# Optimization experiments

Hardware: AMD Instinct MI355X
Metric: run time of the kernel (lower is better)

## Reference

```python
import jax, jax.numpy as jnp
import numpy as np

V, E, H = 32000, 512, 1024
B, T = 16, 256
EPS = 1e-5

def setup_inputs() -> dict:
    key = jax.random.key(0)
    ks = jax.random.split(key, 20)
    s = lambda *shape: 0.02
    inp = {
        'input': jax.random.randint(ks[0], (B, T), 0, V),
        'embd': jax.random.normal(ks[1], (V, E), jnp.float32) * 0.02,
        # layer 0 GRUCell (input E -> H)
        'Wih0': jax.random.normal(ks[2], (3 * H, E), jnp.float32) * 0.02,
        'Whh0': jax.random.normal(ks[3], (3 * H, H), jnp.float32) * 0.02,
        'bih0': jnp.zeros((3 * H,), jnp.float32),
        'bhh0': jnp.zeros((3 * H,), jnp.float32),
        'ln0_w': jnp.ones((H,), jnp.float32),
        'ln0_b': jnp.zeros((H,), jnp.float32),
        # layer 1 GRUCell (H -> H)
        'Wih1': jax.random.normal(ks[4], (3 * H, H), jnp.float32) * 0.02,
        'Whh1': jax.random.normal(ks[5], (3 * H, H), jnp.float32) * 0.02,
        'bih1': jnp.zeros((3 * H,), jnp.float32),
        'bhh1': jnp.zeros((3 * H,), jnp.float32),
        'ln1_w': jnp.ones((H,), jnp.float32),
        'ln1_b': jnp.zeros((H,), jnp.float32),
        # head: Linear(H,H) -> LeakyReLU -> LayerNorm -> Linear(H,V)
        'W1': jax.random.normal(ks[6], (H, H), jnp.float32) * 0.02,
        'b1': jnp.zeros((H,), jnp.float32),
        'ln2_w': jnp.ones((H,), jnp.float32),
        'ln2_b': jnp.zeros((H,), jnp.float32),
        'W2': jax.random.normal(ks[7], (V, H), jnp.float32) * 0.02,
        'b2': jnp.zeros((V,), jnp.float32),
    }
    return inp

def _layernorm(x, w, b):
    m = jnp.mean(x, axis=-1, keepdims=True)
    v = jnp.var(x, axis=-1, keepdims=True)
    return (x - m) * jax.lax.rsqrt(v + EPS) * w + b

def _gru_cell(x, h, Wih, Whh, bih, bhh):
    gi = x @ Wih.T + bih  # [B, 3H]
    gh = h @ Whh.T + bhh
    ir, iz, inn = jnp.split(gi, 3, axis=-1)
    hr, hz, hn = jnp.split(gh, 3, axis=-1)
    r = jax.nn.sigmoid(ir + hr)
    z = jax.nn.sigmoid(iz + hz)
    n = jnp.tanh(inn + r * hn)
    return (1.0 - z) * n + z * h

def reference(input, embd, Wih0, Whh0, bih0, bhh0, ln0_w, ln0_b,
              Wih1, Whh1, bih1, bhh1, ln1_w, ln1_b,
              W1, b1, ln2_w, ln2_b, W2, b2):
    x = embd[input]                      # [B, T, E]
    xT = jnp.swapaxes(x, 0, 1)           # [T, B, E]
    Bn = input.shape[0]
    h0 = jnp.zeros((Bn, H), x.dtype)
    h1 = jnp.zeros((Bn, H), x.dtype)

    def step(carry, xt):
        h0, h1 = carry
        h0 = _layernorm(_gru_cell(xt, h0, Wih0, Whh0, bih0, bhh0), ln0_w, ln0_b)
        h1 = _layernorm(_gru_cell(h0, h1, Wih1, Whh1, bih1, bhh1), ln1_w, ln1_b)
        a = jax.nn.leaky_relu(h1 @ W1.T + b1, negative_slope=0.01)
        a = _layernorm(a, ln2_w, ln2_b)
        logits = a @ W2.T + b2           # [B, V]
        return (h0, h1), logits

    _, outs = jax.lax.scan(step, (h0, h1), xT)   # [T, B, V]
    return jnp.swapaxes(outs, 0, 1)              # [B, T, V]
```

## Files before the change

kernel.cpp:

```cpp
#include <hip/hip_runtime.h>
#include <stdint.h>
#include <math.h>

#define TT 256
#define VOCAB 32000
#define LN_EPS 1e-5

typedef __attribute__((ext_vector_type(8))) short bf16x8;
typedef __attribute__((ext_vector_type(4))) float f32x4;

__device__ __forceinline__ float bf2f(short s) {
  return __uint_as_float(((uint32_t)(uint16_t)s) << 16);
}
__device__ __forceinline__ short f2bf(float f) {
  uint32_t u = __float_as_uint(f);
  u += 0x7fffu + ((u >> 16) & 1u);
  return (short)(u >> 16);
}
__device__ __forceinline__ f32x4 mfma16(bf16x8 a, bf16x8 b, f32x4 c) {
  return __builtin_amdgcn_mfma_f32_16x16x32_bf16(a, b, c, 0, 0, 0);
}

__global__ void k_gi0(const int* __restrict__ input, const float* __restrict__ embd,
                      const float* __restrict__ Wih0, const float* __restrict__ bih0,
                      double* __restrict__ gi0) {
  const int t = blockIdx.x >> 4;
  const int cg = blockIdx.x & 15;
  const int tid = threadIdx.x;
  __shared__ float xs[16][512];
  for (int idx = tid; idx < 16 * 512; idx += 256) {
    const int r = idx >> 9, j = idx & 511;
    const int tok = input[r * TT + t];
    xs[r][j] = embd[(size_t)tok * 512 + j];
  }
  __syncthreads();
  const int row = tid >> 4, ct = tid & 15;
  for (int i = 0; i < 12; ++i) {
    const int c = cg * 192 + ct + 16 * i;
    const float4* wp = (const float4*)(Wih0 + (size_t)c * 512);
    const float4* xp = (const float4*)&xs[row][0];
    double acc = 0.0;
#pragma unroll 8
    for (int j4 = 0; j4 < 128; ++j4) {
      const float4 w = wp[j4];
      const float4 x = xp[j4];
      acc = fma((double)x.x, (double)w.x, acc);
      acc = fma((double)x.y, (double)w.y, acc);
      acc = fma((double)x.z, (double)w.z, acc);
      acc = fma((double)x.w, (double)w.w, acc);
    }
    gi0[((size_t)t * 16 + row) * 3072 + c] = acc + (double)bih0[c];
  }
}

struct SP {
  const float *Whh0, *bhh0, *ln0w, *ln0b;
  const float *Wih1, *Whh1, *bih1, *bhh1, *ln1w, *ln1b;
  const double* gi0;
  double *h0ring, *h1ring;
  float* h1hist;
  int p;
};

__launch_bounds__(512, 2)
__global__ void k_step(SP A) {
  __shared__ double sPre[16 * 16 * 3];
  __shared__ double sM[16], sR[16];
  const int tid = threadIdx.x;
  const int row = tid >> 5;
  const int ks = tid & 31;
  const int bid = blockIdx.x;

  if (bid < 64) {
    const int t = A.p;
    if (t >= TT) return;
    const int col0 = bid * 16;
    double a[32];
    if (t > 0) {
      const double* hp = A.h0ring + (size_t)((t - 1) & 1) * 16384 + row * 1024;
      double s = 0.0, q = 0.0;
#pragma unroll
      for (int g = 0; g < 8; ++g)
#pragma unroll
        for (int u = 0; u < 4; ++u) {
          const double v = hp[g * 128 + ks * 4 + u];
          a[g * 4 + u] = v; s += v; q += v * v;
        }
#pragma unroll
      for (int mk = 1; mk <= 16; mk <<= 1) { s += __shfl_xor(s, mk); q += __shfl_xor(q, mk); }
      const double m = s * (1.0 / 1024.0);
      const double rs = 1.0 / sqrt(q * (1.0 / 1024.0) - m * m + LN_EPS);
      if (ks == 0) { sM[row] = m; sR[row] = rs; }
#pragma unroll
      for (int g = 0; g < 8; ++g) {
        const float4 lw = *(const float4*)(A.ln0w + g * 128 + ks * 4);
        const float4 lb = *(const float4*)(A.ln0b + g * 128 + ks * 4);
        a[g * 4 + 0] = (a[g * 4 + 0] - m) * rs * (double)lw.x + (double)lb.x;
        a[g * 4 + 1] = (a[g * 4 + 1] - m) * rs * (double)lw.y + (double)lb.y;
        a[g * 4 + 2] = (a[g * 4 + 2] - m) * rs * (double)lw.z + (double)lb.z;
        a[g * 4 + 3] = (a[g * 4 + 3] - m) * rs * (double)lw.w + (double)lb.w;
      }
      for (int cc = 0; cc < 16; ++cc) {
        const int c = col0 + cc;
        const float4* pr = (const float4*)(A.Whh0 + (size_t)c * 1024);
        const float4* pz = (const float4*)(A.Whh0 + (size_t)(c + 1024) * 1024);
        const float4* pn = (const float4*)(A.Whh0 + (size_t)(c + 2048) * 1024);
        double ar = 0.0, az = 0.0, an_ = 0.0;
#pragma unroll
        for (int g = 0; g < 8; ++g) {
          const int o = g * 32 + ks;
          const float4 wr = pr[o], wz = pz[o], wn = pn[o];
          ar = fma(a[g*4+0], (double)wr.x, ar); ar = fma(a[g*4+1], (double)wr.y, ar);
          ar = fma(a[g*4+2], (double)wr.z, ar); ar = fma(a[g*4+3], (double)wr.w, ar);
          az = fma(a[g*4+0], (double)wz.x, az); az = fma(a[g*4+1], (double)wz.y, az);
          az = fma(a[g*4+2], (double)wz.z, az); az = fma(a[g*4+3], (double)wz.w, az);
          an_ = fma(a[g*4+0], (double)wn.x, an_); an_ = fma(a[g*4+1], (double)wn.y, an_);
          an_ = fma(a[g*4+2], (double)wn.z, an_); an_ = fma(a[g*4+3], (double)wn.w, an_);
        }
#pragma unroll
        for (int mk = 1; mk <= 16; mk <<= 1) {
          ar += __shfl_xor(ar, mk); az += __shfl_xor(az, mk); an_ += __shfl_xor(an_, mk);
        }
        if (ks == 0) {
          sPre[(row * 16 + cc) * 3 + 0] = ar;
          sPre[(row * 16 + cc) * 3 + 1] = az;
          sPre[(row * 16 + cc) * 3 + 2] = an_;
        }
      }
    } else {
      if (tid < 256) {
        sPre[tid * 3 + 0] = 0.0; sPre[tid * 3 + 1] = 0.0; sPre[tid * 3 + 2] = 0.0;
      }
    }
    __syncthreads();
    if (tid < 256) {
      const int r2 = tid >> 4, cc = tid & 15;
      const int c = col0 + cc;
      const double ghr = sPre[(r2 * 16 + cc) * 3 + 0] + (double)A.bhh0[c];
      const double ghz = sPre[(r2 * 16 + cc) * 3 + 1] + (double)A.bhh0[c + 1024];
      const double ghn = sPre[(r2 * 16 + cc) * 3 + 2] + (double)A.bhh0[c + 2048];
      const double* gp = A.gi0 + ((size_t)t * 16 + r2) * 3072 + c;
      const double gir = gp[0], giz = gp[1024], gin = gp[2048];
      const double rg = 1.0 / (1.0 + exp(-(gir + ghr)));
      const double zg = 1.0 / (1.0 + exp(-(giz + ghz)));
      const double ng = tanh(gin + rg * ghn);
      double hprev = 0.0;
      if (t > 0) {
        const double praw = A.h0ring[(size_t)((t - 1) & 1) * 16384 + r2 * 1024 + c];
        hprev = (praw - sM[r2]) * sR[r2] * (double)A.ln0w[c] + (double)A.ln0b[c];
      }
      A.h0ring[(size_t)(t & 1) * 16384 + r2 * 1024 + c] = (1.0 - zg) * ng + zg * hprev;
    }
  } else {
    const int t = A.p - 1;
    if (t < 0 || t >= TT) return;
    const int col0 = (bid - 64) * 8;
    double a0[32], a1[32];
    {
      const double* hp = A.h0ring + (size_t)(t & 1) * 16384 + row * 1024;
      double s = 0.0, q = 0.0;
#pragma unroll
      for (int g = 0; g < 8; ++g)
#pragma unroll
        for (int u = 0; u < 4; ++u) {
          const double v = hp[g * 128 + ks * 4 + u];
          a0[g * 4 + u] = v; s += v; q += v * v;
        }
#pragma unroll
      for (int mk = 1; mk <= 16; mk <<= 1) { s += __shfl_xor(s, mk); q += __shfl_xor(q, mk); }
      const double m = s * (1.0 / 1024.0);
      const double rs = 1.0 / sqrt(q * (1.0 / 1024.0) - m * m + LN_EPS);
#pragma unroll
      for (int g = 0; g < 8; ++g) {
        const float4 lw = *(const float4*)(A.ln0w + g * 128 + ks * 4);
        const float4 lb = *(const float4*)(A.ln0b + g * 128 + ks * 4);
        a0[g * 4 + 0] = (a0[g * 4 + 0] - m) * rs * (double)lw.x + (double)lb.x;
        a0[g * 4 + 1] = (a0[g * 4 + 1] - m) * rs * (double)lw.y + (double)lb.y;
        a0[g * 4 + 2] = (a0[g * 4 + 2] - m) * rs * (double)lw.z + (double)lb.z;
        a0[g * 4 + 3] = (a0[g * 4 + 3] - m) * rs * (double)lw.w + (double)lb.w;
      }
    }
    if (t > 0) {
      const double* hp = A.h1ring + (size_t)((t - 1) & 1) * 16384 + row * 1024;
      double s = 0.0, q = 0.0;
#pragma unroll
      for (int g = 0; g < 8; ++g)
#pragma unroll
        for (int u = 0; u < 4; ++u) {
          const double v = hp[g * 128 + ks * 4 + u];
          a1[g * 4 + u] = v; s += v; q += v * v;
        }
#pragma unroll
      for (int mk = 1; mk <= 16; mk <<= 1) { s += __shfl_xor(s, mk); q += __shfl_xor(q, mk); }
      const double m = s * (1.0 / 1024.0);
      const double rs = 1.0 / sqrt(q * (1.0 / 1024.0) - m * m + LN_EPS);
      if (ks == 0) { sM[row] = m; sR[row] = rs; }
#pragma unroll
      for (int g = 0; g < 8; ++g) {
        const float4 lw = *(const float4*)(A.ln1w + g * 128 + ks * 4);
        const float4 lb = *(const float4*)(A.ln1b + g * 128 + ks * 4);
        a1[g * 4 + 0] = (a1[g * 4 + 0] - m) * rs * (double)lw.x + (double)lb.x;
        a1[g * 4 + 1] = (a1[g * 4 + 1] - m) * rs * (double)lw.y + (double)lb.y;
        a1[g * 4 + 2] = (a1[g * 4 + 2] - m) * rs * (double)lw.z + (double)lb.z;
        a1[g * 4 + 3] = (a1[g * 4 + 3] - m) * rs * (double)lw.w + (double)lb.w;
      }
    } else {
#pragma unroll
      for (int j = 0; j < 32; ++j) a1[j] = 0.0;
    }
    for (int cc = 0; cc < 8; ++cc) {
      const int c = col0 + cc;
      const float4* ir = (const float4*)(A.Wih1 + (size_t)c * 1024);
      const float4* iz = (const float4*)(A.Wih1 + (size_t)(c + 1024) * 1024);
      const float4* in_ = (const float4*)(A.Wih1 + (size_t)(c + 2048) * 1024);
      const float4* hr = (const float4*)(A.Whh1 + (size_t)c * 1024);
      const float4* hz = (const float4*)(A.Whh1 + (size_t)(c + 1024) * 1024);
      const float4* hn = (const float4*)(A.Whh1 + (size_t)(c + 2048) * 1024);
      double sIr = 0.0, sIz = 0.0, sIn = 0.0, sHr = 0.0, sHz = 0.0, sHn = 0.0;
#pragma unroll
      for (int g = 0; g < 8; ++g) {
        const int o = g * 32 + ks;
        const float4 w0 = ir[o], w1 = iz[o], w2 = in_[o];
        const float4 w3 = hr[o], w4 = hz[o], w5 = hn[o];
        sIr = fma(a0[g*4+0], (double)w0.x, sIr); sIr = fma(a0[g*4+1], (double)w0.y, sIr);
        sIr = fma(a0[g*4+2], (double)w0.z, sIr); sIr = fma(a0[g*4+3], (double)w0.w, sIr);
        sIz = fma(a0[g*4+0], (double)w1.x, sIz); sIz = fma(a0[g*4+1], (double)w1.y, sIz);
        sIz = fma(a0[g*4+2], (double)w1.z, sIz); sIz = fma(a0[g*4+3], (double)w1.w, sIz);
        sIn = fma(a0[g*4+0], (double)w2.x, sIn); sIn = fma(a0[g*4+1], (double)w2.y, sIn);
        sIn = fma(a0[g*4+2], (double)w2.z, sIn); sIn = fma(a0[g*4+3], (double)w2.w, sIn);
        sHr = fma(a1[g*4+0], (double)w3.x, sHr); sHr = fma(a1[g*4+1], (double)w3.y, sHr);
        sHr = fma(a1[g*4+2], (double)w3.z, sHr); sHr = fma(a1[g*4+3], (double)w3.w, sHr);
        sHz = fma(a1[g*4+0], (double)w4.x, sHz); sHz = fma(a1[g*4+1], (double)w4.y, sHz);
        sHz = fma(a1[g*4+2], (double)w4.z, sHz); sHz = fma(a1[g*4+3], (double)w4.w, sHz);
        sHn = fma(a1[g*4+0], (double)w5.x, sHn); sHn = fma(a1[g*4+1], (double)w5.y, sHn);
        sHn = fma(a1[g*4+2], (double)w5.z, sHn); sHn = fma(a1[g*4+3], (double)w5.w, sHn);
      }
#pragma unroll
      for (int mk = 1; mk <= 16; mk <<= 1) {
        sIr += __shfl_xor(sIr, mk); sIz += __shfl_xor(sIz, mk); sIn += __shfl_xor(sIn, mk);
        sHr += __shfl_xor(sHr, mk); sHz += __shfl_xor(sHz, mk); sHn += __shfl_xor(sHn, mk);
      }
      if (ks == 0) {
        double* pp = &sPre[(row * 8 + cc) * 6];
        pp[0] = sIr; pp[1] = sIz; pp[2] = sIn; pp[3] = sHr; pp[4] = sHz; pp[5] = sHn;
      }
    }
    __syncthreads();
    if (tid < 128) {
      const int r2 = tid >> 3, cc = tid & 7;
      const int c = col0 + cc;
      const double* pp = &sPre[(r2 * 8 + cc) * 6];
      const double gir = pp[0] + (double)A.bih1[c];
      const double giz = pp[1] + (double)A.bih1[c + 1024];
      const double gin = pp[2] + (double)A.bih1[c + 2048];
      const double ghr = pp[3] + (double)A.bhh1[c];
      const double ghz = pp[4] + (double)A.bhh1[c + 1024];
      const double ghn = pp[5] + (double)A.bhh1[c + 2048];
      const double rg = 1.0 / (1.0 + exp(-(gir + ghr)));
      const double zg = 1.0 / (1.0 + exp(-(giz + ghz)));
      const double ng = tanh(gin + rg * ghn);
      double hprev = 0.0;
      if (t > 0) {
        const double praw = A.h1ring[(size_t)((t - 1) & 1) * 16384 + r2 * 1024 + c];
        hprev = (praw - sM[r2]) * sR[r2] * (double)A.ln1w[c] + (double)A.ln1b[c];
      }
      const double hnew = (1.0 - zg) * ng + zg * hprev;
      A.h1ring[(size_t)(t & 1) * 16384 + r2 * 1024 + c] = hnew;
      A.h1hist[((size_t)t * 16 + r2) * 1024 + c] = (float)hnew;
    }
  }
}

__launch_bounds__(512, 2)
__global__ void k_headpre(const float* __restrict__ h1hist, const float* __restrict__ ln1w,
                          const float* __restrict__ ln1b, const float* __restrict__ W1,
                          const float* __restrict__ b1, short* __restrict__ araw) {
  const int tid = threadIdx.x;
  const int row = tid >> 5, ks = tid & 31;
  const size_t m = (size_t)blockIdx.x * 16 + row;
  const float* hp = h1hist + m * 1024;
  float a[32];
  float s = 0.f, q = 0.f;
#pragma unroll
  for (int g = 0; g < 8; ++g) {
    const float4 v = *(const float4*)(hp + g * 128 + ks * 4);
    a[g*4+0] = v.x; a[g*4+1] = v.y; a[g*4+2] = v.z; a[g*4+3] = v.w;
    s += v.x + v.y + v.z + v.w;
    q += v.x * v.x + v.y * v.y + v.z * v.z + v.w * v.w;
  }
#pragma unroll
  for (int mk = 1; mk <= 16; mk <<= 1) { s += __shfl_xor(s, mk); q += __shfl_xor(q, mk); }
  const float mn = s * (1.f / 1024.f);
  const float rs = rsqrtf(q * (1.f / 1024.f) - mn * mn + 1e-5f);
#pragma unroll
  for (int g = 0; g < 8; ++g) {
    const float4 lw = *(const float4*)(ln1w + g * 128 + ks * 4);
    const float4 lb = *(const float4*)(ln1b + g * 128 + ks * 4);
    a[g*4+0] = (a[g*4+0] - mn) * rs * lw.x + lb.x;
    a[g*4+1] = (a[g*4+1] - mn) * rs * lw.y + lb.y;
    a[g*4+2] = (a[g*4+2] - mn) * rs * lw.z + lb.z;
    a[g*4+3] = (a[g*4+3] - mn) * rs * lw.w + lb.w;
  }
  for (int c = 0; c < 1024; ++c) {
    const float4* wp = (const float4*)(W1 + (size_t)c * 1024);
    float acc = 0.f;
#pragma unroll
    for (int g = 0; g < 8; ++g) {
      const float4 w = wp[g * 32 + ks];
      acc = fmaf(a[g*4+0], w.x, acc); acc = fmaf(a[g*4+1], w.y, acc);
      acc = fmaf(a[g*4+2], w.z, acc); acc = fmaf(a[g*4+3], w.w, acc);
    }
#pragma unroll
    for (int mk = 1; mk <= 16; mk <<= 1) acc += __shfl_xor(acc, mk);
    if (ks == 0) {
      const float y = acc + b1[c];
      araw[m * 1024 + c] = f2bf(y > 0.f ? y : 0.01f * y);
    }
  }
}

__global__ void k_head(const short* __restrict__ araw, const float* __restrict__ W2,
                       const float* __restrict__ ln2w, const float* __restrict__ ln2b,
                       const float* __restrict__ b2, float* __restrict__ C) {
  __shared__ __align__(16) short As[128 * 64];
  __shared__ __align__(16) short Bs[128 * 64];
  __shared__ float rowm[128], rowr[128];
  __shared__ float lnw_s[1024], lnb_s[1024];
  __shared__ float ps[256], pq[256];
  const int tid = threadIdx.x;
  const long brow = (long)blockIdx.y * 128;
  const long bcol = (long)blockIdx.x * 128;

  for (int i = tid; i < 1024; i += 256) { lnw_s[i] = ln2w[i]; lnb_s[i] = ln2b[i]; }
  {
    const int r2 = tid >> 1, hf = tid & 1;
    const short* ap = araw + (brow + r2) * 1024 + hf * 512;
    float s = 0.f, q = 0.f;
    for (int j = 0; j < 512; j += 8) {
      const bf16x8 v = *(const bf16x8*)(ap + j);
#pragma unroll
      for (int e = 0; e < 8; ++e) { const float x = bf2f(v[e]); s += x; q += x * x; }
    }
    ps[tid] = s; pq[tid] = q;
  }
  __syncthreads();
  if (tid < 128) {
    const float s = ps[2 * tid] + ps[2 * tid + 1];
    const float q = pq[2 * tid] + pq[2 * tid + 1];
    const float m = s * (1.f / 1024.f);
    rowm[tid] = m;
    rowr[tid] = rsqrtf(q * (1.f / 1024.f) - m * m + 1e-5f);
  }
  __syncthreads();

  const int l = tid & 63;
  const int w = tid >> 6;
  const int wm = w >> 1, wn = w & 1;
  const int lane15 = l & 15, lgrp = l >> 4;
  f32x4 zero4 = {0.f, 0.f, 0.f, 0.f};
  f32x4 acc[4][4];
#pragma unroll
  for (int ri = 0; ri < 4; ++ri)
#pragma unroll
    for (int ci = 0; ci < 4; ++ci) acc[ri][ci] = zero4;

  for (int k0 = 0; k0 < 1024; k0 += 64) {
    __syncthreads();
#pragma unroll
    for (int i = 0; i < 4; ++i) {
      const int c = tid + i * 256;
      const int r = c >> 3, cc = c & 7;
      const int k = k0 + cc * 8;
      {
        const bf16x8 v = *(const bf16x8*)(araw + (brow + r) * 1024 + k);
        const float mm = rowm[r], rr = rowr[r];
        bf16x8 o;
#pragma unroll
        for (int e = 0; e < 8; ++e)
          o[e] = f2bf((bf2f(v[e]) - mm) * rr * lnw_s[k + e] + lnb_s[k + e]);
        *(bf16x8*)&As[r * 64 + cc * 8] = o;
      }
      {
        const float4* bp = (const float4*)(W2 + (bcol + r) * 1024 + k);
        const float4 v0 = bp[0], v1 = bp[1];
        bf16x8 o;
        o[0] = f2bf(v0.x); o[1] = f2bf(v0.y); o[2] = f2bf(v0.z); o[3] = f2bf(v0.w);
        o[4] = f2bf(v1.x); o[5] = f2bf(v1.y); o[6] = f2bf(v1.z); o[7] = f2bf(v1.w);
        *(bf16x8*)&Bs[r * 64 + cc * 8] = o;
      }
    }
    __syncthreads();
#pragma unroll
    for (int kk = 0; kk < 2; ++kk) {
      const int ko = kk * 32 + lgrp * 8;
      bf16x8 av[4], bv[4];
#pragma unroll
      for (int ri = 0; ri < 4; ++ri) av[ri] = *(const bf16x8*)&As[(wm * 64 + ri * 16 + lane15) * 64 + ko];
#pragma unroll
      for (int ci = 0; ci < 4; ++ci) bv[ci] = *(const bf16x8*)&Bs[(wn * 64 + ci * 16 + lane15) * 64 + ko];
#pragma unroll
      for (int ri = 0; ri < 4; ++ri)
#pragma unroll
        for (int ci = 0; ci < 4; ++ci) acc[ri][ci] = mfma16(av[ri], bv[ci], acc[ri][ci]);
    }
  }
#pragma unroll
  for (int ri = 0; ri < 4; ++ri)
#pragma unroll
    for (int ci = 0; ci < 4; ++ci)
#pragma unroll
      for (int i = 0; i < 4; ++i) {
        const long mrow = brow + wm * 64 + ri * 16 + lgrp * 4 + i;
        const long ncol = bcol + wn * 64 + ci * 16 + lane15;
        const int tq = (int)(mrow >> 4), b = (int)(mrow & 15);
        C[(size_t)b * TT * VOCAB + (size_t)tq * VOCAB + ncol] = acc[ri][ci][i] + b2[ncol];
      }
}

extern "C" void kernel_launch(void* const* d_in, const int* in_sizes, int n_in,
                              void* d_out, int out_size, void* d_ws, size_t ws_size,
                              hipStream_t stream) {
  const int* input = (const int*)d_in[0];
  const float* embd = (const float*)d_in[1];
  const float* Wih0 = (const float*)d_in[2];
  const float* Whh0 = (const float*)d_in[3];
  const float* bih0 = (const float*)d_in[4];
  const float* bhh0 = (const float*)d_in[5];
  const float* ln0w = (const float*)d_in[6];
  const float* ln0b = (const float*)d_in[7];
  const float* Wih1 = (const float*)d_in[8];
  const float* Whh1 = (const float*)d_in[9];
  const float* bih1 = (const float*)d_in[10];
  const float* bhh1 = (const float*)d_in[11];
  const float* ln1w = (const float*)d_in[12];
  const float* ln1b = (const float*)d_in[13];
  const float* W1 = (const float*)d_in[14];
  const float* b1 = (const float*)d_in[15];
  const float* ln2w = (const float*)d_in[16];
  const float* ln2b = (const float*)d_in[17];
  const float* W2 = (const float*)d_in[18];
  const float* b2 = (const float*)d_in[19];
  float* out = (float*)d_out;

  char* ws = (char*)d_ws;
  size_t off = 0;
  auto alloc = [&](size_t bytes) -> char* {
    char* p = ws + off;
    off = (off + bytes + 255) & ~(size_t)255;
    return p;
  };
  double* h0ring = (double*)alloc(2ull * 16 * 1024 * 8);
  double* h1ring = (double*)alloc(2ull * 16 * 1024 * 8);
  float* h1hist = (float*)alloc(4096ull * 1024 * 4);
  short* araw = (short*)alloc(4096ull * 1024 * 2);

  double* gi0 = (double*)d_out;

  k_gi0<<<4096, 256, 0, stream>>>(input, embd, Wih0, bih0, gi0);

  SP A;
  A.Whh0 = Whh0; A.bhh0 = bhh0; A.ln0w = ln0w; A.ln0b = ln0b;
  A.Wih1 = Wih1; A.Whh1 = Whh1; A.bih1 = bih1; A.bhh1 = bhh1;
  A.ln1w = ln1w; A.ln1b = ln1b;
  A.gi0 = gi0; A.h0ring = h0ring; A.h1ring = h1ring; A.h1hist = h1hist;
  for (int p = 0; p <= TT; ++p) {
    A.p = p;
    k_step<<<192, 512, 0, stream>>>(A);
  }

  k_headpre<<<256, 512, 0, stream>>>(h1hist, ln1w, ln1b, W1, b1, araw);

  k_head<<<dim3(250, 32), 256, 0, stream>>>(araw, W2, ln2w, ln2b, b2, out);
}
```

Measured before the change: 15.92 ms.

## Replace per-step kernel launches with persistent kernel and grid-wide atomic barrier

```diff
diff --git a/kernel.cpp b/kernel.cpp
--- a/kernel.cpp
+++ b/kernel.cpp
@@ -5,6 +5,7 @@
 #define TT 256
 #define VOCAB 32000
 #define LN_EPS 1e-5
+#define NBLK 192
 
 typedef __attribute__((ext_vector_type(8))) short bf16x8;
 typedef __attribute__((ext_vector_type(4))) float f32x4;
@@ -59,11 +60,11 @@
   const double* gi0;
   double *h0ring, *h1ring;
   float* h1hist;
-  int p;
+  int* bar;
 };
 
-__launch_bounds__(512, 2)
-__global__ void k_step(SP A) {
+__launch_bounds__(512, 1)
+__global__ void k_recur(SP A) {
   __shared__ double sPre[16 * 16 * 3];
   __shared__ double sM[16], sR[16];
   const int tid = threadIdx.x;
@@ -71,203 +72,219 @@
   const int ks = tid & 31;
   const int bid = blockIdx.x;
 
-  if (bid < 64) {
-    const int t = A.p;
-    if (t >= TT) return;
-    const int col0 = bid * 16;
-    double a[32];
-    if (t > 0) {
-      const double* hp = A.h0ring + (size_t)((t - 1) & 1) * 16384 + row * 1024;
-      double s = 0.0, q = 0.0;
-#pragma unroll
-      for (int g = 0; g < 8; ++g)
-#pragma unroll
-        for (int u = 0; u < 4; ++u) {
-          const double v = hp[g * 128 + ks * 4 + u];
-          a[g * 4 + u] = v; s += v; q += v * v;
-        }
-#pragma unroll
-      for (int mk = 1; mk <= 16; mk <<= 1) { s += __shfl_xor(s, mk); q += __shfl_xor(q, mk); }
-      const double m = s * (1.0 / 1024.0);
-      const double rs = 1.0 / sqrt(q * (1.0 / 1024.0) - m * m + LN_EPS);
-      if (ks == 0) { sM[row] = m; sR[row] = rs; }
-#pragma unroll
-      for (int g = 0; g < 8; ++g) {
-        const float4 lw = *(const float4*)(A.ln0w + g * 128 + ks * 4);
-        const float4 lb = *(const float4*)(A.ln0b + g * 128 + ks * 4);
-        a[g * 4 + 0] = (a[g * 4 + 0] - m) * rs * (double)lw.x + (double)lb.x;
-        a[g * 4 + 1] = (a[g * 4 + 1] - m) * rs * (double)lw.y + (double)lb.y;
-        a[g * 4 + 2] = (a[g * 4 + 2] - m) * rs * (double)lw.z + (double)lb.z;
-        a[g * 4 + 3] = (a[g * 4 + 3] - m) * rs * (double)lw.w + (double)lb.w;
-      }
-      for (int cc = 0; cc < 16; ++cc) {
-        const int c = col0 + cc;
-        const float4* pr = (const float4*)(A.Whh0 + (size_t)c * 1024);
-        const float4* pz = (const float4*)(A.Whh0 + (size_t)(c + 1024) * 1024);
-        const float4* pn = (const float4*)(A.Whh0 + (size_t)(c + 2048) * 1024);
-        double ar = 0.0, az = 0.0, an_ = 0.0;
-#pragma unroll
-        for (int g = 0; g < 8; ++g) {
-          const int o = g * 32 + ks;
-          const float4 wr = pr[o], wz = pz[o], wn = pn[o];
-          ar = fma(a[g*4+0], (double)wr.x, ar); ar = fma(a[g*4+1], (double)wr.y, ar);
-          ar = fma(a[g*4+2], (double)wr.z, ar); ar = fma(a[g*4+3], (double)wr.w, ar);
-          az = fma(a[g*4+0], (double)wz.x, az); az = fma(a[g*4+1], (double)wz.y, az);
-          az = fma(a[g*4+2], (double)wz.z, az); az = fma(a[g*4+3], (double)wz.w, az);
-          an_ = fma(a[g*4+0], (double)wn.x, an_); an_ = fma(a[g*4+1], (double)wn.y, an_);
-          an_ = fma(a[g*4+2], (double)wn.z, an_); an_ = fma(a[g*4+3], (double)wn.w, an_);
-        }
-#pragma unroll
-        for (int mk = 1; mk <= 16; mk <<= 1) {
-          ar += __shfl_xor(ar, mk); az += __shfl_xor(az, mk); an_ += __shfl_xor(an_, mk);
-        }
-        if (ks == 0) {
-          sPre[(row * 16 + cc) * 3 + 0] = ar;
-          sPre[(row * 16 + cc) * 3 + 1] = az;
-          sPre[(row * 16 + cc) * 3 + 2] = an_;
+  for (int p = 0; p <= TT; ++p) {
+    if (bid < 64) {
+      const int t = p;
+      if (t < TT) {
+        const int col0 = bid * 16;
+        double a[32];
+        if (t > 0) {
+          const double* hp = A.h0ring + (size_t)((t - 1) & 1) * 16384 + row * 1024;
+          double s = 0.0, q = 0.0;
+#pragma unroll
+          for (int g = 0; g < 8; ++g)
+#pragma unroll
+            for (int u = 0; u < 4; ++u) {
+              const double v = hp[g * 128 + ks * 4 + u];
+              a[g * 4 + u] = v; s += v; q += v * v;
+            }
+#pragma unroll
+          for (int mk = 1; mk <= 16; mk <<= 1) { s += __shfl_xor(s, mk); q += __shfl_xor(q, mk); }
+          const double m = s * (1.0 / 1024.0);
+          const double rs = 1.0 / sqrt(q * (1.0 / 1024.0) - m * m + LN_EPS);
+          if (ks == 0) { sM[row] = m; sR[row] = rs; }
+#pragma unroll
+          for (int g = 0; g < 8; ++g) {
+            const float4 lw = *(const float4*)(A.ln0w + g * 128 + ks * 4);
+            const float4 lb = *(const float4*)(A.ln0b + g * 128 + ks * 4);
+            a[g * 4 + 0] = (a[g * 4 + 0] - m) * rs * (double)lw.x + (double)lb.x;
+            a[g * 4 + 1] = (a[g * 4 + 1] - m) * rs * (double)lw.y + (double)lb.y;
+            a[g * 4 + 2] = (a[g * 4 + 2] - m) * rs * (double)lw.z + (double)lb.z;
+            a[g * 4 + 3] = (a[g * 4 + 3] - m) * rs * (double)lw.w + (double)lb.w;
+          }
+          for (int cc = 0; cc < 16; ++cc) {
+            const int c = col0 + cc;
+            const float4* pr = (const float4*)(A.Whh0 + (size_t)c * 1024);
+            const float4* pz = (const float4*)(A.Whh0 + (size_t)(c + 1024) * 1024);
+            const float4* pn = (const float4*)(A.Whh0 + (size_t)(c + 2048) * 1024);
+            double ar = 0.0, az = 0.0, an_ = 0.0;
+#pragma unroll
+            for (int g = 0; g < 8; ++g) {
+              const int o = g * 32 + ks;
+              const float4 wr = pr[o], wz = pz[o], wn = pn[o];
+              ar = fma(a[g*4+0], (double)wr.x, ar); ar = fma(a[g*4+1], (double)wr.y, ar);
+              ar = fma(a[g*4+2], (double)wr.z, ar); ar = fma(a[g*4+3], (double)wr.w, ar);
+              az = fma(a[g*4+0], (double)wz.x, az); az = fma(a[g*4+1], (double)wz.y, az);
+              az = fma(a[g*4+2], (double)wz.z, az); az = fma(a[g*4+3], (double)wz.w, az);
+              an_ = fma(a[g*4+0], (double)wn.x, an_); an_ = fma(a[g*4+1], (double)wn.y, an_);
+              an_ = fma(a[g*4+2], (double)wn.z, an_); an_ = fma(a[g*4+3], (double)wn.w, an_);
+            }
+#pragma unroll
+            for (int mk = 1; mk <= 16; mk <<= 1) {
+              ar += __shfl_xor(ar, mk); az += __shfl_xor(az, mk); an_ += __shfl_xor(an_, mk);
+            }
+            if (ks == 0) {
+              sPre[(row * 16 + cc) * 3 + 0] = ar;
+              sPre[(row * 16 + cc) * 3 + 1] = az;
+              sPre[(row * 16 + cc) * 3 + 2] = an_;
+            }
+          }
+        } else {
+          if (tid < 256) {
+            sPre[tid * 3 + 0] = 0.0; sPre[tid * 3 + 1] = 0.0; sPre[tid * 3 + 2] = 0.0;
+          }
+        }
+        __syncthreads();
+        if (tid < 256) {
+          const int r2 = tid >> 4, cc = tid & 15;
+          const int c = col0 + cc;
+          const double ghr = sPre[(r2 * 16 + cc) * 3 + 0] + (double)A.bhh0[c];
+          const double ghz = sPre[(r2 * 16 + cc) * 3 + 1] + (double)A.bhh0[c + 1024];
+          const double ghn = sPre[(r2 * 16 + cc) * 3 + 2] + (double)A.bhh0[c + 2048];
+          const double* gp = A.gi0 + ((size_t)t * 16 + r2) * 3072 + c;
+          const double gir = gp[0], giz = gp[1024], gin = gp[2048];
+          const double rg = 1.0 / (1.0 + exp(-(gir + ghr)));
+          const double zg = 1.0 / (1.0 + exp(-(giz + ghz)));
+          const double ng = tanh(gin + rg * ghn);
+          double hprev = 0.0;
+          if (t > 0) {
+            const double praw = A.h0ring[(size_t)((t - 1) & 1) * 16384 + r2 * 1024 + c];
+            hprev = (praw - sM[r2]) * sR[r2] * (double)A.ln0w[c] + (double)A.ln0b[c];
+          }
+          A.h0ring[(size_t)(t & 1) * 16384 + r2 * 1024 + c] = (1.0 - zg) * ng + zg * hprev;
         }
       }
     } else {
-      if (tid < 256) {
-        sPre[tid * 3 + 0] = 0.0; sPre[tid * 3 + 1] = 0.0; sPre[tid * 3 + 2] = 0.0;
-      }
-    }
+      const int t = p - 1;
+      if (t >= 0 && t < TT) {
+        const int col0 = (bid - 64) * 8;
+        double a0[32], a1[32];
+        {
+          const double* hp = A.h0ring + (size_t)(t & 1) * 16384 + row * 1024;
+          double s = 0.0, q = 0.0;
+#pragma unroll
+          for (int g = 0; g < 8; ++g)
+#pragma unroll
+            for (int u = 0; u < 4; ++u) {
+              const double v = hp[g * 128 + ks * 4 + u];
+              a0[g * 4 + u] = v; s += v; q += v * v;
+            }
+#pragma unroll
+          for (int mk = 1; mk <= 16; mk <<= 1) { s += __shfl_xor(s, mk); q += __shfl_xor(q, mk); }
+          const double m = s * (1.0 / 1024.0);
+          const double rs = 1.0 / sqrt(q * (1.0 / 1024.0) - m * m + LN_EPS);
+#pragma unroll
+          for (int g = 0; g < 8; ++g) {
+            const float4 lw = *(const float4*)(A.ln0w + g * 128 + ks * 4);
+            const float4 lb = *(const float4*)(A.ln0b + g * 128 + ks * 4);
+            a0[g * 4 + 0] = (a0[g * 4 + 0] - m) * rs * (double)lw.x + (double)lb.x;
+            a0[g * 4 + 1] = (a0[g * 4 + 1] - m) * rs * (double)lw.y + (double)lb.y;
+            a0[g * 4 + 2] = (a0[g * 4 + 2] - m) * rs * (double)lw.z + (double)lb.z;
+            a0[g * 4 + 3] = (a0[g * 4 + 3] - m) * rs * (double)lw.w + (double)lb.w;
+          }
+        }
+        if (t > 0) {
+          const double* hp = A.h1ring + (size_t)((t - 1) & 1) * 16384 + row * 1024;
+          double s = 0.0, q = 0.0;
+#pragma unroll
+          for (int g = 0; g < 8; ++g)
+#pragma unroll
+            for (int u = 0; u < 4; ++u) {
+              const double v = hp[g * 128 + ks * 4 + u];
+              a1[g * 4 + u] = v; s += v; q += v * v;
+            }
+#pragma unroll
+          for (int mk = 1; mk <= 16; mk <<= 1) { s += __shfl_xor(s, mk); q += __shfl_xor(q, mk); }
+          const double m = s * (1.0 / 1024.0);
+          const double rs = 1.0 / sqrt(q * (1.0 / 1024.0) - m * m + LN_EPS);
+          if (ks == 0) { sM[row] = m; sR[row] = rs; }
+#pragma unroll
+          for (int g = 0; g < 8; ++g) {
+            const float4 lw = *(const float4*)(A.ln1w + g * 128 + ks * 4);
+            const float4 lb = *(const float4*)(A.ln1b + g * 128 + ks * 4);
+            a1[g * 4 + 0] = (a1[g * 4 + 0] - m) * rs * (double)lw.x + (double)lb.x;
+            a1[g * 4 + 1] = (a1[g * 4 + 1] - m) * rs * (double)lw.y + (double)lb.y;
+            a1[g * 4 + 2] = (a1[g * 4 + 2] - m) * rs * (double)lw.z + (double)lb.z;
+            a1[g * 4 + 3] = (a1[g * 4 + 3] - m) * rs * (double)lw.w + (double)lb.w;
+          }
+        } else {
+#pragma unroll
+          for (int j = 0; j < 32; ++j) a1[j] = 0.0;
+        }
+        for (int cc = 0; cc < 8; ++cc) {
+          const int c = col0 + cc;
+          const float4* ir = (const float4*)(A.Wih1 + (size_t)c * 1024);
+          const float4* iz = (const float4*)(A.Wih1 + (size_t)(c + 1024) * 1024);
+          const float4* in_ = (const float4*)(A.Wih1 + (size_t)(c + 2048) * 1024);
+          const float4* hr = (const float4*)(A.Whh1 + (size_t)c * 1024);
+          const float4* hz = (const float4*)(A.Whh1 + (size_t)(c + 1024) * 1024);
+          const float4* hn = (const float4*)(A.Whh1 + (size_t)(c + 2048) * 1024);
+          double sIr = 0.0, sIz = 0.0, sIn = 0.0, sHr = 0.0, sHz = 0.0, sHn = 0.0;
+#pragma unroll
+          for (int g = 0; g < 8; ++g) {
+            const int o = g * 32 + ks;
+            const float4 w0 = ir[o], w1 = iz[o], w2 = in_[o];
+            const float4 w3 = hr[o], w4 = hz[o], w5 = hn[o];
+            sIr = fma(a0[g*4+0], (double)w0.x, sIr); sIr = fma(a0[g*4+1], (double)w0.y, sIr);
+            sIr = fma(a0[g*4+2], (double)w0.z, sIr); sIr = fma(a0[g*4+3], (double)w0.w, sIr);
+            sIz = fma(a0[g*4+0], (double)w1.x, sIz); sIz = fma(a0[g*4+1], (double)w1.y, sIz);
+            sIz = fma(a0[g*4+2], (double)w1.z, sIz); sIz = fma(a0[g*4+3], (double)w1.w, sIz);
+            sIn = fma(a0[g*4+0], (double)w2.x, sIn); sIn = fma(a0[g*4+1], (double)w2.y, sIn);
+            sIn = fma(a0[g*4+2], (double)w2.z, sIn); sIn = fma(a0[g*4+3], (double)w2.w, sIn);
+            sHr = fma(a1[g*4+0], (double)w3.x, sHr); sHr = fma(a1[g*4+1], (double)w3.y, sHr);
+            sHr = fma(a1[g*4+2], (double)w3.z, sHr); sHr = fma(a1[g*4+3], (double)w3.w, sHr);
+            sHz = fma(a1[g*4+0], (double)w4.x, sHz); sHz = fma(a1[g*4+1], (double)w4.y, sHz);
+            sHz = fma(a1[g*4+2], (double)w4.z, sHz); sHz = fma(a1[g*4+3], (double)w4.w, sHz);
+            sHn = fma(a1[g*4+0], (double)w5.x, sHn); sHn = fma(a1[g*4+1], (double)w5.y, sHn);
+            sHn = fma(a1[g*4+2], (double)w5.z, sHn); sHn = fma(a1[g*4+3], (double)w5.w, sHn);
+          }
+#pragma unroll
+          for (int mk = 1; mk <= 16; mk <<= 1) {
+            sIr += __shfl_xor(sIr, mk); sIz += __shfl_xor(sIz, mk); sIn += __shfl_xor(sIn, mk);
+            sHr += __shfl_xor(sHr, mk); sHz += __shfl_xor(sHz, mk); sHn += __shfl_xor(sHn, mk);
+          }
+          if (ks == 0) {
+            double* pp = &sPre[(row * 8 + cc) * 6];
+            pp[0] = sIr; pp[1] = sIz; pp[2] = sIn; pp[3] = sHr; pp[4] = sHz; pp[5] = sHn;
+          }
+        }
+        __syncthreads();
+        if (tid < 128) {
+          const int r2 = tid >> 3, cc = tid & 7;
+          const int c = col0 + cc;
+          const double* pp = &sPre[(r2 * 8 + cc) * 6];
+          const double gir = pp[0] + (double)A.bih1[c];
+          const double giz = pp[1] + (double)A.bih1[c + 1024];
+          const double gin = pp[2] + (double)A.bih1[c + 2048];
+          const double ghr = pp[3] + (double)A.bhh1[c];
+          const double ghz = pp[4] + (double)A.bhh1[c + 1024];
+          const double ghn = pp[5] + (double)A.bhh1[c + 2048];
+          const double rg = 1.0 / (1.0 + exp(-(gir + ghr)));
+          const double zg = 1.0 / (1.0 + exp(-(giz + ghz)));
+          const double ng = tanh(gin + rg * ghn);
+          double hprev = 0.0;
+          if (t > 0) {
+            const double praw = A.h1ring[(size_t)((t - 1) & 1) * 16384 + r2 * 1024 + c];
+            hprev = (praw - sM[r2]) * sR[r2] * (double)A.ln1w[c] + (double)A.ln1b[c];
+          }
+          const double hnew = (1.0 - zg) * ng + zg * hprev;
+          A.h1ring[(size_t)(t & 1) * 16384 + r2 * 1024 + c] = hnew;
+          A.h1hist[((size_t)t * 16 + r2) * 1024 + c] = (float)hnew;
+        }
+      }
+    }
+
     __syncthreads();
-    if (tid < 256) {
-      const int r2 = tid >> 4, cc = tid & 15;
-      const int c = col0 + cc;
-      const double ghr = sPre[(r2 * 16 + cc) * 3 + 0] + (double)A.bhh0[c];
-      const double ghz = sPre[(r2 * 16 + cc) * 3 + 1] + (double)A.bhh0[c + 1024];
-      const double ghn = sPre[(r2 * 16 + cc) * 3 + 2] + (double)A.bhh0[c + 2048];
-      const double* gp = A.gi0 + ((size_t)t * 16 + r2) * 3072 + c;
-      const double gir = gp[0], giz = gp[1024], gin = gp[2048];
-      const double rg = 1.0 / (1.0 + exp(-(gir + ghr)));
-      const double zg = 1.0 / (1.0 + exp(-(giz + ghz)));
-      const double ng = tanh(gin + rg * ghn);
-      double hprev = 0.0;
-      if (t > 0) {
-        const double praw = A.h0ring[(size_t)((t - 1) & 1) * 16384 + r2 * 1024 + c];
-        hprev = (praw - sM[r2]) * sR[r2] * (double)A.ln0w[c] + (double)A.ln0b[c];
-      }
-      A.h0ring[(size_t)(t & 1) * 16384 + r2 * 1024 + c] = (1.0 - zg) * ng + zg * hprev;
-    }
-  } else {
-    const int t = A.p - 1;
-    if (t < 0 || t >= TT) return;
-    const int col0 = (bid - 64) * 8;
-    double a0[32], a1[32];
-    {
-      const double* hp = A.h0ring + (size_t)(t & 1) * 16384 + row * 1024;
-      double s = 0.0, q = 0.0;
-#pragma unroll
-      for (int g = 0; g < 8; ++g)
-#pragma unroll
-        for (int u = 0; u < 4; ++u) {
-          const double v = hp[g * 128 + ks * 4 + u];
-          a0[g * 4 + u] = v; s += v; q += v * v;
-        }
-#pragma unroll
-      for (int mk = 1; mk <= 16; mk <<= 1) { s += __shfl_xor(s, mk); q += __shfl_xor(q, mk); }
-      const double m = s * (1.0 / 1024.0);
-      const double rs = 1.0 / sqrt(q * (1.0 / 1024.0) - m * m + LN_EPS);
-#pragma unroll
-      for (int g = 0; g < 8; ++g) {
-        const float4 lw = *(const float4*)(A.ln0w + g * 128 + ks * 4);
-        const float4 lb = *(const float4*)(A.ln0b + g * 128 + ks * 4);
-        a0[g * 4 + 0] = (a0[g * 4 + 0] - m) * rs * (double)lw.x + (double)lb.x;
-        a0[g * 4 + 1] = (a0[g * 4 + 1] - m) * rs * (double)lw.y + (double)lb.y;
-        a0[g * 4 + 2] = (a0[g * 4 + 2] - m) * rs * (double)lw.z + (double)lb.z;
-        a0[g * 4 + 3] = (a0[g * 4 + 3] - m) * rs * (double)lw.w + (double)lb.w;
-      }
-    }
-    if (t > 0) {
-      const double* hp = A.h1ring + (size_t)((t - 1) & 1) * 16384 + row * 1024;
-      double s = 0.0, q = 0.0;
-#pragma unroll
-      for (int g = 0; g < 8; ++g)
-#pragma unroll
-        for (int u = 0; u < 4; ++u) {
-          const double v = hp[g * 128 + ks * 4 + u];
-          a1[g * 4 + u] = v; s += v; q += v * v;
-        }
-#pragma unroll
-      for (int mk = 1; mk <= 16; mk <<= 1) { s += __shfl_xor(s, mk); q += __shfl_xor(q, mk); }
-      const double m = s * (1.0 / 1024.0);
-      const double rs = 1.0 / sqrt(q * (1.0 / 1024.0) - m * m + LN_EPS);
-      if (ks == 0) { sM[row] = m; sR[row] = rs; }
-#pragma unroll
-      for (int g = 0; g < 8; ++g) {
-        const float4 lw = *(const float4*)(A.ln1w + g * 128 + ks * 4);
-        const float4 lb = *(const float4*)(A.ln1b + g * 128 + ks * 4);
-        a1[g * 4 + 0] = (a1[g * 4 + 0] - m) * rs * (double)lw.x + (double)lb.x;
-        a1[g * 4 + 1] = (a1[g * 4 + 1] - m) * rs * (double)lw.y + (double)lb.y;
-        a1[g * 4 + 2] = (a1[g * 4 + 2] - m) * rs * (double)lw.z + (double)lb.z;
-        a1[g * 4 + 3] = (a1[g * 4 + 3] - m) * rs * (double)lw.w + (double)lb.w;
-      }
-    } else {
-#pragma unroll
-      for (int j = 0; j < 32; ++j) a1[j] = 0.0;
-    }
-    for (int cc = 0; cc < 8; ++cc) {
-      const int c = col0 + cc;
-      const float4* ir = (const float4*)(A.Wih1 + (size_t)c * 1024);
-      const float4* iz = (const float4*)(A.Wih1 + (size_t)(c + 1024) * 1024);
-      const float4* in_ = (const float4*)(A.Wih1 + (size_t)(c + 2048) * 1024);
-      const float4* hr = (const float4*)(A.Whh1 + (size_t)c * 1024);
-      const float4* hz = (const float4*)(A.Whh1 + (size_t)(c + 1024) * 1024);
-      const float4* hn = (const float4*)(A.Whh1 + (size_t)(c + 2048) * 1024);
-      double sIr = 0.0, sIz = 0.0, sIn = 0.0, sHr = 0.0, sHz = 0.0, sHn = 0.0;
-#pragma unroll
-      for (int g = 0; g < 8; ++g) {
-        const int o = g * 32 + ks;
-        const float4 w0 = ir[o], w1 = iz[o], w2 = in_[o];
-        const float4 w3 = hr[o], w4 = hz[o], w5 = hn[o];
-        sIr = fma(a0[g*4+0], (double)w0.x, sIr); sIr = fma(a0[g*4+1], (double)w0.y, sIr);
-        sIr = fma(a0[g*4+2], (double)w0.z, sIr); sIr = fma(a0[g*4+3], (double)w0.w, sIr);
-        sIz = fma(a0[g*4+0], (double)w1.x, sIz); sIz = fma(a0[g*4+1], (double)w1.y, sIz);
-        sIz = fma(a0[g*4+2], (double)w1.z, sIz); sIz = fma(a0[g*4+3], (double)w1.w, sIz);
-        sIn = fma(a0[g*4+0], (double)w2.x, sIn); sIn = fma(a0[g*4+1], (double)w2.y, sIn);
-        sIn = fma(a0[g*4+2], (double)w2.z, sIn); sIn = fma(a0[g*4+3], (double)w2.w, sIn);
-        sHr = fma(a1[g*4+0], (double)w3.x, sHr); sHr = fma(a1[g*4+1], (double)w3.y, sHr);
-        sHr = fma(a1[g*4+2], (double)w3.z, sHr); sHr = fma(a1[g*4+3], (double)w3.w, sHr);
-        sHz = fma(a1[g*4+0], (double)w4.x, sHz); sHz = fma(a1[g*4+1], (double)w4.y, sHz);
-        sHz = fma(a1[g*4+2], (double)w4.z, sHz); sHz = fma(a1[g*4+3], (double)w4.w, sHz);
-        sHn = fma(a1[g*4+0], (double)w5.x, sHn); sHn = fma(a1[g*4+1], (double)w5.y, sHn);
-        sHn = fma(a1[g*4+2], (double)w5.z, sHn); sHn = fma(a1[g*4+3], (double)w5.w, sHn);
-      }
-#pragma unroll
-      for (int mk = 1; mk <= 16; mk <<= 1) {
-        sIr += __shfl_xor(sIr, mk); sIz += __shfl_xor(sIz, mk); sIn += __shfl_xor(sIn, mk);
-        sHr += __shfl_xor(sHr, mk); sHz += __shfl_xor(sHz, mk); sHn += __shfl_xor(sHn, mk);
-      }
-      if (ks == 0) {
-        double* pp = &sPre[(row * 8 + cc) * 6];
-        pp[0] = sIr; pp[1] = sIz; pp[2] = sIn; pp[3] = sHr; pp[4] = sHz; pp[5] = sHn;
-      }
+    if (tid == 0) {
+      __threadfence();
+      __hip_atomic_fetch_add(A.bar, 1, __ATOMIC_ACQ_REL, __HIP_MEMORY_SCOPE_AGENT);
+      const int target = NBLK * (p + 1);
+      while (__hip_atomic_load(A.bar, __ATOMIC_ACQUIRE, __HIP_MEMORY_SCOPE_AGENT) < target) {
+        __builtin_amdgcn_s_sleep(8);
+      }
+      __threadfence();
     }
     __syncthreads();
-    if (tid < 128) {
-      const int r2 = tid >> 3, cc = tid & 7;
-      const int c = col0 + cc;
-      const double* pp = &sPre[(r2 * 8 + cc) * 6];
-      const double gir = pp[0] + (double)A.bih1[c];
-      const double giz = pp[1] + (double)A.bih1[c + 1024];
-      const double gin = pp[2] + (double)A.bih1[c + 2048];
-      const double ghr = pp[3] + (double)A.bhh1[c];
-      const double ghz = pp[4] + (double)A.bhh1[c + 1024];
-      const double ghn = pp[5] + (double)A.bhh1[c + 2048];
-      const double rg = 1.0 / (1.0 + exp(-(gir + ghr)));
-      const double zg = 1.0 / (1.0 + exp(-(giz + ghz)));
-      const double ng = tanh(gin + rg * ghn);
-      double hprev = 0.0;
-      if (t > 0) {
-        const double praw = A.h1ring[(size_t)((t - 1) & 1) * 16384 + r2 * 1024 + c];
-        hprev = (praw - sM[r2]) * sR[r2] * (double)A.ln1w[c] + (double)A.ln1b[c];
-      }
-      const double hnew = (1.0 - zg) * ng + zg * hprev;
-      A.h1ring[(size_t)(t & 1) * 16384 + r2 * 1024 + c] = hnew;
-      A.h1hist[((size_t)t * 16 + r2) * 1024 + c] = (float)hnew;
-    }
   }
 }
 
@@ -453,6 +470,9 @@
   double* h1ring = (double*)alloc(2ull * 16 * 1024 * 8);
   float* h1hist = (float*)alloc(4096ull * 1024 * 4);
   short* araw = (short*)alloc(4096ull * 1024 * 2);
+  int* bar = (int*)alloc(256);
+
+  hipMemsetAsync(bar, 0, 256, stream);
 
   double* gi0 = (double*)d_out;
 
@@ -463,10 +483,8 @@
   A.Wih1 = Wih1; A.Whh1 = Whh1; A.bih1 = bih1; A.bhh1 = bhh1;
   A.ln1w = ln1w; A.ln1b = ln1b;
   A.gi0 = gi0; A.h0ring = h0ring; A.h1ring = h1ring; A.h1hist = h1hist;
-  for (int p = 0; p <= TT; ++p) {
-    A.p = p;
-    k_step<<<192, 512, 0, stream>>>(A);
-  }
+  A.bar = bar;
+  k_recur<<<NBLK, 512, 0, stream>>>(A);
 
   k_headpre<<<256, 512, 0, stream>>>(h1hist, ln1w, ln1b, W1, b1, araw);
 
```

Measured after the change: 26.92 ms. 69.0% more time.
